# Performance work log

Hardware: AMD Instinct MI355X
Metric: run time of the kernel (lower is better)

Reference implementation:

```python
import jax, jax.numpy as jnp
import numpy as np

EPS = 1e-6
LAMBDA_INIT = 0.8

def rmsnorm(x, g):
    return x * jax.lax.rsqrt(jnp.mean(x * x, axis=-1, keepdims=True) + EPS) * g

def diff_attention(q_in, kv_in, Wq, Wk, Wv, Wo, lq1, lk1, lq2, lk2, causal):
    # q_in: [B,T,D], kv_in: [B,S,D]; Wq/Wk: [D, H*2*hs], Wv: [D, H*hs], Wo: [H*hs, D]
    B, T, _ = q_in.shape
    S = kv_in.shape[1]
    H, hs = lq1.shape
    q = (q_in @ Wq).reshape(B, T, H, 2, hs)
    k = (kv_in @ Wk).reshape(B, S, H, 2, hs)
    v = (kv_in @ Wv).reshape(B, S, H, hs)
    q1, q2 = q[..., 0, :], q[..., 1, :]
    k1, k2 = k[..., 0, :], k[..., 1, :]
    scale = 1.0 / np.sqrt(hs).astype(np.float32)
    a1 = jnp.einsum('bthd,bshd->bhts', q1, k1) * scale  # [B,H,T,S]
    a2 = jnp.einsum('bthd,bshd->bhts', q2, k2) * scale
    if causal:
        mask = jnp.tril(jnp.ones((T, S), dtype=bool))
        neg = jnp.asarray(-1e9, a1.dtype)
        a1 = jnp.where(mask, a1, neg)
        a2 = jnp.where(mask, a2, neg)
    s1 = jax.nn.softmax(a1, axis=-1)
    s2 = jax.nn.softmax(a2, axis=-1)
    lam = jnp.exp(jnp.sum(lq1 * lk1, -1)) - jnp.exp(jnp.sum(lq2 * lk2, -1)) + LAMBDA_INIT  # [H]
    attn = s1 - lam[None, :, None, None] * s2
    o = jnp.einsum('bhts,bshd->bthd', attn, v)  # [B,T,H,hs]
    # per-head RMSNorm (no affine) scaled by (1 - lambda_init), per Diff Transformer
    o = o * jax.lax.rsqrt(jnp.mean(o * o, -1, keepdims=True) + EPS) * (1.0 - LAMBDA_INIT)
    return o.reshape(B, T, H * hs) @ Wo

def swiglu(x, W1, W2, W3):
    return (jax.nn.silu(x @ W1) * (x @ W2)) @ W3

def setup_inputs():
    B, T, D, H, hs = 4, 1024, 1024, 16, 64
    Dff = 4 * D
    ks = jax.random.split(jax.random.key(0), 24)
    w = lambda i, shape, s=0.02: (jax.random.normal(ks[i], shape, jnp.float32) * s)
    return {
        'x': jax.random.normal(ks[0], (B, T, D), jnp.float32),
        'encoder_output': jax.random.normal(ks[1], (B, T, D), jnp.float32),
        'Wq_s': w(2, (D, H * 2 * hs)), 'Wk_s': w(3, (D, H * 2 * hs)),
        'Wv_s': w(4, (D, H * hs)), 'Wo_s': w(5, (H * hs, D)),
        'lq1_s': w(6, (H, hs), 0.1), 'lk1_s': w(7, (H, hs), 0.1),
        'lq2_s': w(8, (H, hs), 0.1), 'lk2_s': w(9, (H, hs), 0.1),
        'Wq_c': w(10, (D, H * 2 * hs)), 'Wk_c': w(11, (D, H * 2 * hs)),
        'Wv_c': w(12, (D, H * hs)), 'Wo_c': w(13, (H * hs, D)),
        'lq1_c': w(14, (H, hs), 0.1), 'lk1_c': w(15, (H, hs), 0.1),
        'lq2_c': w(16, (H, hs), 0.1), 'lk2_c': w(17, (H, hs), 0.1),
        'g_rms': jnp.ones((D,), jnp.float32),
        'W1': w(18, (D, Dff)), 'W2': w(19, (D, Dff)), 'W3': w(20, (Dff, D)),
    }

def reference(x, encoder_output, Wq_s, Wk_s, Wv_s, Wo_s, lq1_s, lk1_s, lq2_s, lk2_s,
              Wq_c, Wk_c, Wv_c, Wo_c, lq1_c, lk1_c, lq2_c, lk2_c,
              g_rms, W1, W2, W3):
    # dropout prob 0.0 -> identity (eval/reference mode)
    h = rmsnorm(x, g_rms)
    h = diff_attention(h, h, Wq_s, Wk_s, Wv_s, Wo_s, lq1_s, lk1_s, lq2_s, lk2_s, causal=True) + h
    h = diff_attention(h, encoder_output, Wq_c, Wk_c, Wv_c, Wo_c, lq1_c, lk1_c, lq2_c, lk2_c, causal=False)
    h = h + h  # faithful to source: out = dropout(out) + out after cross-attention
    h = swiglu(rmsnorm(h, g_rms), W1, W2, W3) + h
    return h
```

## Files before the change

kernel.cpp:

```cpp
#include <hip/hip_runtime.h>

typedef __attribute__((ext_vector_type(8))) short s16x8;
typedef __attribute__((ext_vector_type(4))) float f32x4;
typedef unsigned short u16;

__device__ __forceinline__ float bu2f(u16 u) {
    union { unsigned int i; float f; } x; x.i = ((unsigned int)u) << 16; return x.f;
}
__device__ __forceinline__ u16 f2bu(float f) {
    union { float f; unsigned int i; } x; x.f = f;
    unsigned int r = x.i + 0x7fffu + ((x.i >> 16) & 1u);
    return (u16)(r >> 16);
}

__device__ __forceinline__ void gld_lds16(const void* g, void* l) {
    __builtin_amdgcn_global_load_lds(
        (const __attribute__((address_space(1))) unsigned int*)g,
        (__attribute__((address_space(3))) unsigned int*)l, 16, 0, 0);
}
#define WAIT_VM0()   asm volatile("s_waitcnt vmcnt(0)" ::: "memory")
#define WAIT_LGKM0() asm volatile("s_waitcnt lgkmcnt(0)" ::: "memory")
#define RAW_BARRIER() asm volatile("s_barrier" ::: "memory")
#define MEMBAR()     asm volatile("" ::: "memory")

__global__ __launch_bounds__(256)
void transpose4_k(const float* s0, const float* s1, const float* s2, const float* s3,
                  u16* d0, u16* d1, u16* d2, u16* d3, int R, int C) {
    const float* src = blockIdx.z == 0 ? s0 : blockIdx.z == 1 ? s1 : blockIdx.z == 2 ? s2 : s3;
    u16* dst = blockIdx.z == 0 ? d0 : blockIdx.z == 1 ? d1 : blockIdx.z == 2 ? d2 : d3;
    __shared__ u16 t[32][33];
    int bx = blockIdx.x * 32, by = blockIdx.y * 32;
    int x = bx + threadIdx.x;
#pragma unroll
    for (int k = 0; k < 4; ++k)
        t[threadIdx.y + k * 8][threadIdx.x] = f2bu(src[(size_t)(by + threadIdx.y + k * 8) * C + x]);
    __syncthreads();
    int x2 = by + threadIdx.x;
#pragma unroll
    for (int k = 0; k < 4; ++k)
        dst[(size_t)(bx + threadIdx.y + k * 8) * R + x2] = t[threadIdx.x][threadIdx.y + k * 8];
}

__global__ __launch_bounds__(256)
void convert_k(const float* __restrict__ a, u16* __restrict__ o, int n4) {
    int i = blockIdx.x * 256 + threadIdx.x;
    if (i >= n4) return;
    float4 v = ((const float4*)a)[i];
    ushort4 u;
    u.x = f2bu(v.x); u.y = f2bu(v.y); u.z = f2bu(v.z); u.w = f2bu(v.w);
    ((ushort4*)o)[i] = u;
}

__global__ __launch_bounds__(256)
void rmsnorm_k(const float* __restrict__ x, const float* __restrict__ g, u16* __restrict__ y) {
    const int row = blockIdx.x, tid = threadIdx.x;
    float4 v = ((const float4*)(x + (size_t)row * 1024))[tid];
    float ss = v.x * v.x + v.y * v.y + v.z * v.z + v.w * v.w;
#pragma unroll
    for (int off = 32; off; off >>= 1) ss += __shfl_xor(ss, off, 64);
    __shared__ float red[4];
    if ((tid & 63) == 0) red[tid >> 6] = ss;
    __syncthreads();
    float tot = red[0] + red[1] + red[2] + red[3];
    float sc = rsqrtf(tot * (1.f / 1024.f) + 1e-6f);
    float4 gv = ((const float4*)g)[tid];
    ushort4 o;
    o.x = f2bu(v.x * sc * gv.x);
    o.y = f2bu(v.y * sc * gv.y);
    o.z = f2bu(v.z * sc * gv.z);
    o.w = f2bu(v.w * sc * gv.w);
    ((ushort4*)(y + (size_t)row * 1024))[tid] = o;
}

__global__ __launch_bounds__(256)
void silumul_k(const u16* __restrict__ a, const u16* __restrict__ b, u16* __restrict__ o, int n4) {
    int i = blockIdx.x * 256 + threadIdx.x;
    if (i >= n4) return;
    ushort4 ua = ((const ushort4*)a)[i], ub = ((const ushort4*)b)[i];
    ushort4 uo;
    {
        float v = bu2f(ua.x); uo.x = f2bu(v / (1.f + __expf(-v)) * bu2f(ub.x));
        v = bu2f(ua.y); uo.y = f2bu(v / (1.f + __expf(-v)) * bu2f(ub.y));
        v = bu2f(ua.z); uo.z = f2bu(v / (1.f + __expf(-v)) * bu2f(ub.z));
        v = bu2f(ua.w); uo.w = f2bu(v / (1.f + __expf(-v)) * bu2f(ub.w));
    }
    ((ushort4*)o)[i] = uo;
}

template <int TM>
__global__ __launch_bounds__(256, 2)
void gemm_bt(const u16* __restrict__ A, const u16* __restrict__ Bt, void* __restrict__ C,
             const void* __restrict__ res, int M, int N, int K, int mode) {
    constexpr int MI = TM / 32;
    __shared__ u16 sA[2][TM * 32];
    __shared__ u16 sB[2][128 * 32];
    const int tid = threadIdx.x;
    const int w = tid >> 6, lane = tid & 63, q4 = lane >> 4, l16 = lane & 15;
    const int m0 = blockIdx.y * TM, n0 = blockIdx.x * 128;
    const int wm = (w >> 1) * (TM / 2), wn = (w & 1) * 64;

    const f32x4 fzero = {0.f, 0.f, 0.f, 0.f};
    f32x4 acc[MI][4];
#pragma unroll
    for (int i = 0; i < MI; ++i)
#pragma unroll
        for (int j = 0; j < 4; ++j) acc[i][j] = fzero;

    const int r0 = tid >> 2, c0 = (tid & 3) * 8;

    auto stage = [&](int buf, int k0) {
        gld_lds16(A + (size_t)(m0 + r0) * K + k0 + c0, &sA[buf][tid * 8]);
        if (TM == 128)
            gld_lds16(A + (size_t)(m0 + 64 + r0) * K + k0 + c0, &sA[buf][(256 + tid) * 8]);
        gld_lds16(Bt + (size_t)(n0 + r0) * K + k0 + c0, &sB[buf][tid * 8]);
        gld_lds16(Bt + (size_t)(n0 + 64 + r0) * K + k0 + c0, &sB[buf][(256 + tid) * 8]);
    };

    const int nk = K >> 5;
    stage(0, 0);
    for (int it = 0; it < nk; ++it) {
        WAIT_VM0();
        RAW_BARRIER();
        if (it + 1 < nk) stage((it + 1) & 1, (it + 1) * 32);
        const int buf = it & 1;
        s16x8 af[MI], bfr[4];
#pragma unroll
        for (int i = 0; i < MI; ++i) af[i] = *(const s16x8*)&sA[buf][(wm + i * 16 + l16) * 32 + q4 * 8];
#pragma unroll
        for (int j = 0; j < 4; ++j) bfr[j] = *(const s16x8*)&sB[buf][(wn + j * 16 + l16) * 32 + q4 * 8];
#pragma unroll
        for (int i = 0; i < MI; ++i)
#pragma unroll
            for (int j = 0; j < 4; ++j)
                acc[i][j] = __builtin_amdgcn_mfma_f32_16x16x32_bf16(af[i], bfr[j], acc[i][j], 0, 0, 0);
        MEMBAR();
    }

    const size_t QBSZ = (size_t)4096 * 2048;
    const size_t FSZ  = (size_t)4096 * 4096;
#pragma unroll
    for (int i = 0; i < MI; ++i)
#pragma unroll
        for (int j = 0; j < 4; ++j)
#pragma unroll
            for (int r = 0; r < 4; ++r) {
                int m = m0 + wm + i * 16 + q4 * 4 + r;
                int n = n0 + wn + j * 16 + l16;
                float v = acc[i][j][r];
                if (mode == 0) {
                    ((u16*)C)[(size_t)m * N + n] = f2bu(v);
                } else if (mode == 1) {
                    ((u16*)C)[(size_t)m * N + n] = f2bu(v + bu2f(((const u16*)res)[(size_t)m * N + n]));
                } else if (mode == 2) {
                    ((float*)C)[(size_t)m * N + n] = 2.f * v;
                } else if (mode == 4) {
                    ((float*)C)[(size_t)m * N + n] = v + ((const float*)res)[(size_t)m * N + n];
                } else if (mode == 5) {
                    if (n < 2048) ((u16*)C)[(size_t)m * 2048 + n] = f2bu(v);
                    else if (n < 4096) ((u16*)C)[QBSZ + (size_t)m * 2048 + (n - 2048)] = f2bu(v);
                    else {
                        int nn = n - 4096, hh = nn >> 6, d = nn & 63, b = m >> 10, s = m & 1023;
                        ((u16*)C)[2 * QBSZ + ((size_t)((b * 16 + hh) * 64 + d)) * 1024 + s] = f2bu(v);
                    }
                } else if (mode == 6) {
                    if (n < 2048) ((u16*)C)[(size_t)m * 2048 + n] = f2bu(v);
                    else {
                        int nn = n - 2048, hh = nn >> 6, d = nn & 63, b = m >> 10, s = m & 1023;
                        ((u16*)C)[QBSZ + ((size_t)((b * 16 + hh) * 64 + d)) * 1024 + s] = f2bu(v);
                    }
                } else {
                    if (n < 4096) ((u16*)C)[(size_t)m * 4096 + n] = f2bu(v);
                    else ((u16*)C)[FSZ + (size_t)m * 4096 + (n - 4096)] = f2bu(v);
                }
            }
}

template <bool CAUSAL>
__global__ __launch_bounds__(256, 2)
void diff_flash(const u16* __restrict__ Q, const u16* __restrict__ Kg, const u16* __restrict__ Vt,
                u16* __restrict__ O, const float* __restrict__ lq1, const float* __restrict__ lk1,
                const float* __restrict__ lq2, const float* __restrict__ lk2, int T, int S) {
    __shared__ u16 sK1[2][64 * 64];
    __shared__ u16 sK2[2][64 * 64];
    __shared__ u16 sV[2][64 * 64];
    __shared__ u16 sP[4][16 * 64];

    const int tid = threadIdx.x;
    const int w = tid >> 6, lane = tid & 63, q4 = lane >> 4, l16 = lane & 15;
    const int h = blockIdx.x, b = blockIdx.y;
    const int zt = CAUSAL ? (gridDim.z - 1 - blockIdx.z) : blockIdx.z;
    const int t0 = zt * 64;
    const f32x4 fzero = {0.f, 0.f, 0.f, 0.f};

    float d1 = 0.f, d2 = 0.f;
    for (int d = 0; d < 64; ++d) {
        d1 += lq1[h * 64 + d] * lk1[h * 64 + d];
        d2 += lq2[h * 64 + d] * lk2[h * 64 + d];
    }
    const float lam = __expf(d1) - __expf(d2) + 0.8f;

    s16x8 qf[2][2];
    {
        const size_t qrow = (size_t)(b * T + t0 + w * 16 + l16) * 2048 + h * 128;
#pragma unroll
        for (int c = 0; c < 2; ++c)
#pragma unroll
            for (int kk = 0; kk < 2; ++kk)
                qf[c][kk] = *(const s16x8*)&Q[qrow + c * 64 + kk * 32 + q4 * 8];
    }

    f32x4 o1[4], o2[4];
    float ms1 = -1e30f, ls1 = 0.f, ms2 = -1e30f, ls2 = 0.f;
#pragma unroll
    for (int jn = 0; jn < 4; ++jn) { o1[jn] = fzero; o2[jn] = fzero; }

    const int ntiles = CAUSAL ? (zt + 1) : (S / 64);
    const int rk = tid >> 3;
    const int ckk = (((tid & 7) - rk) & 7) * 8;

    auto stage = [&](int buf, int s0) {
        const size_t kb = (size_t)(b * S + s0 + rk) * 2048 + h * 128;
        gld_lds16(&Kg[kb + ckk], &sK1[buf][tid * 8]);
        gld_lds16(&Kg[kb + (size_t)32 * 2048 + ckk], &sK1[buf][(256 + tid) * 8]);
        gld_lds16(&Kg[kb + 64 + ckk], &sK2[buf][tid * 8]);
        gld_lds16(&Kg[kb + (size_t)32 * 2048 + 64 + ckk], &sK2[buf][(256 + tid) * 8]);
        const size_t vb = (size_t)((b * 16 + h) * 64 + rk) * 1024 + s0;
        gld_lds16(&Vt[vb + ckk], &sV[buf][tid * 8]);
        gld_lds16(&Vt[vb + (size_t)32 * 1024 + ckk], &sV[buf][(256 + tid) * 8]);
    };

    u16* const sPw = sP[w];
    const int slot0 = ((0 * 4 + q4 + l16) & 7) * 8;
    const int slot1 = ((1 * 4 + q4 + l16) & 7) * 8;

    stage(0, 0);
    for (int it = 0; it < ntiles; ++it) {
        WAIT_VM0();
        RAW_BARRIER();
        if (it + 1 < ntiles) stage((it + 1) & 1, (it + 1) * 64);
        const int buf = it & 1, s0 = it * 64;
        const bool diag = CAUSAL && (it == ntiles - 1);

        s16x8 vf[4][2];
#pragma unroll
        for (int jn = 0; jn < 4; ++jn) {
            vf[jn][0] = *(const s16x8*)&sV[buf][(jn * 16 + l16) * 64 + slot0];
            vf[jn][1] = *(const s16x8*)&sV[buf][(jn * 16 + l16) * 64 + slot1];
        }

        auto comp_step = [&](const u16* sK, const s16x8* qkk, float& m, float& l, f32x4* o) {
            f32x4 sc[4];
#pragma unroll
            for (int js = 0; js < 4; ++js) sc[js] = fzero;
#pragma unroll
            for (int js = 0; js < 4; ++js) {
                s16x8 kf0 = *(const s16x8*)&sK[(js * 16 + l16) * 64 + slot0];
                sc[js] = __builtin_amdgcn_mfma_f32_16x16x32_bf16(kf0, qkk[0], sc[js], 0, 0, 0);
                s16x8 kf1 = *(const s16x8*)&sK[(js * 16 + l16) * 64 + slot1];
                sc[js] = __builtin_amdgcn_mfma_f32_16x16x32_bf16(kf1, qkk[1], sc[js], 0, 0, 0);
            }
            float p[4][4];
#pragma unroll
            for (int js = 0; js < 4; ++js)
#pragma unroll
                for (int r = 0; r < 4; ++r) {
                    float v = sc[js][r] * 0.125f;
                    if (diag && (s0 + js * 16 + q4 * 4 + r > t0 + w * 16 + l16)) v = -1e9f;
                    p[js][r] = v;
                }
            float mx = p[0][0];
#pragma unroll
            for (int js = 0; js < 4; ++js)
#pragma unroll
                for (int r = 0; r < 4; ++r) mx = fmaxf(mx, p[js][r]);
            mx = fmaxf(mx, __shfl_xor(mx, 16, 64));
            mx = fmaxf(mx, __shfl_xor(mx, 32, 64));
            float mn = fmaxf(m, mx);
            float alpha = __expf(m - mn);
            m = mn;
            float rs = 0.f;
#pragma unroll
            for (int js = 0; js < 4; ++js)
#pragma unroll
                for (int r = 0; r < 4; ++r) { p[js][r] = __expf(p[js][r] - mn); rs += p[js][r]; }
            rs += __shfl_xor(rs, 16, 64);
            rs += __shfl_xor(rs, 32, 64);
            l = l * alpha + rs;
#pragma unroll
            for (int jn = 0; jn < 4; ++jn) o[jn] *= alpha;
#pragma unroll
            for (int js = 0; js < 4; ++js) {
                ushort4 pk;
                pk.x = f2bu(p[js][0]); pk.y = f2bu(p[js][1]);
                pk.z = f2bu(p[js][2]); pk.w = f2bu(p[js][3]);
                int sl = ((js * 2 + (q4 >> 1) + l16) & 7) * 8 + (q4 & 1) * 4;
                *(ushort4*)&sPw[l16 * 64 + sl] = pk;
            }
            WAIT_LGKM0();
            s16x8 pb0 = *(const s16x8*)&sPw[l16 * 64 + slot0];
            s16x8 pb1 = *(const s16x8*)&sPw[l16 * 64 + slot1];
#pragma unroll
            for (int jn = 0; jn < 4; ++jn) {
                o[jn] = __builtin_amdgcn_mfma_f32_16x16x32_bf16(vf[jn][0], pb0, o[jn], 0, 0, 0);
                o[jn] = __builtin_amdgcn_mfma_f32_16x16x32_bf16(vf[jn][1], pb1, o[jn], 0, 0, 0);
            }
            MEMBAR();
        };
        comp_step(sK1[buf], qf[0], ms1, ls1, o1);
        comp_step(sK2[buf], qf[1], ms2, ls2, o2);
    }

    const float inv1 = 1.f / ls1, inv2 = lam / ls2;
    float val[4][4];
    float ss = 0.f;
#pragma unroll
    for (int jn = 0; jn < 4; ++jn)
#pragma unroll
        for (int r = 0; r < 4; ++r) {
            float v = o1[jn][r] * inv1 - o2[jn][r] * inv2;
            val[jn][r] = v;
            ss += v * v;
        }
    ss += __shfl_xor(ss, 16, 64);
    ss += __shfl_xor(ss, 32, 64);
    const float scl = rsqrtf(ss * (1.f / 64.f) + 1e-6f) * 0.2f;
    const size_t orow = (size_t)(b * T + t0 + w * 16 + l16) * 1024 + h * 64;
#pragma unroll
    for (int jn = 0; jn < 4; ++jn) {
        ushort4 ov;
        ov.x = f2bu(val[jn][0] * scl); ov.y = f2bu(val[jn][1] * scl);
        ov.z = f2bu(val[jn][2] * scl); ov.w = f2bu(val[jn][3] * scl);
        *(ushort4*)&O[orow + jn * 16 + q4 * 4] = ov;
    }
}

extern "C" void kernel_launch(void* const* d_in, const int* in_sizes, int n_in,
                              void* d_out, int out_size, void* d_ws, size_t ws_size,
                              hipStream_t stream) {
    (void)in_sizes; (void)n_in; (void)out_size; (void)ws_size;
    const float* x     = (const float*)d_in[0];
    const float* enc   = (const float*)d_in[1];
    const float* Wq_s  = (const float*)d_in[2];
    const float* Wk_s  = (const float*)d_in[3];
    const float* Wv_s  = (const float*)d_in[4];
    const float* Wo_s  = (const float*)d_in[5];
    const float* lq1_s = (const float*)d_in[6];
    const float* lk1_s = (const float*)d_in[7];
    const float* lq2_s = (const float*)d_in[8];
    const float* lk2_s = (const float*)d_in[9];
    const float* Wq_c  = (const float*)d_in[10];
    const float* Wk_c  = (const float*)d_in[11];
    const float* Wv_c  = (const float*)d_in[12];
    const float* Wo_c  = (const float*)d_in[13];
    const float* lq1_c = (const float*)d_in[14];
    const float* lk1_c = (const float*)d_in[15];
    const float* lq2_c = (const float*)d_in[16];
    const float* lk2_c = (const float*)d_in[17];
    const float* g_rms = (const float*)d_in[18];
    const float* W1    = (const float*)d_in[19];
    const float* W2    = (const float*)d_in[20];
    const float* W3    = (const float*)d_in[21];

    char* ws = (char*)d_ws;
    size_t off = 0;
    auto ab = [&](size_t elems) -> u16* { u16* p = (u16*)(ws + off); off += elems * 2; return p; };
    u16* WqkvTs = ab((size_t)5120 * 1024);
    u16* WoTs   = ab((size_t)1024 * 1024);
    u16* WqTc   = ab((size_t)2048 * 1024);
    u16* WkvTc  = ab((size_t)3072 * 1024);
    u16* WoTc   = ab((size_t)1024 * 1024);
    u16* W12T   = ab((size_t)8192 * 1024);
    u16* W3T    = ab((size_t)1024 * 4096);
    char* pool = ws + off;
    u16* h0   = ab((size_t)4096 * 1024);
    u16* encb = ab((size_t)4096 * 1024);
    u16* Qb   = ab((size_t)4096 * 2048);
    u16* Kb   = ab((size_t)4096 * 2048);
    u16* Vt   = ab((size_t)4096 * 1024);
    u16* Ob   = ab((size_t)4096 * 1024);
    u16* fa   = (u16*)pool;
    u16* fb   = (u16*)(pool + (size_t)4096 * 4096 * 2);
    u16* h1   = ab((size_t)4096 * 1024);
    float* h2 = (float*)(ws + off); off += (size_t)4096 * 1024 * 4;
    u16* rn   = ab((size_t)4096 * 1024);

    dim3 tb(32, 8);
    transpose4_k<<<dim3(64, 32, 4), tb, 0, stream>>>(
        Wq_s, Wk_s, Wq_c, Wk_c,
        WqkvTs, WqkvTs + (size_t)2048 * 1024, WqTc, WkvTc, 1024, 2048);
    transpose4_k<<<dim3(32, 32, 4), tb, 0, stream>>>(
        Wv_s, Wo_s, Wv_c, Wo_c,
        WqkvTs + (size_t)4096 * 1024, WoTs, WkvTc + (size_t)2048 * 1024, WoTc, 1024, 1024);
    transpose4_k<<<dim3(128, 32, 2), tb, 0, stream>>>(
        W1, W2, W1, W2, W12T, W12T + (size_t)4096 * 1024, W12T, W12T, 1024, 4096);
    transpose4_k<<<dim3(32, 128, 1), tb, 0, stream>>>(W3, W3, W3, W3, W3T, W3T, W3T, W3T, 4096, 1024);

    rmsnorm_k<<<4096, 256, 0, stream>>>(x, g_rms, h0);
    convert_k<<<4096, 256, 0, stream>>>(enc, encb, 4096 * 1024 / 4);

    gemm_bt<128><<<dim3(40, 32), 256, 0, stream>>>(h0, WqkvTs, Qb, nullptr, 4096, 5120, 1024, 5);
    diff_flash<true><<<dim3(16, 4, 16), 256, 0, stream>>>(Qb, Kb, Vt, Ob, lq1_s, lk1_s, lq2_s, lk2_s, 1024, 1024);
    gemm_bt<64><<<dim3(8, 64), 256, 0, stream>>>(Ob, WoTs, h1, h0, 4096, 1024, 1024, 1);

    gemm_bt<128><<<dim3(16, 32), 256, 0, stream>>>(h1, WqTc, Qb, nullptr, 4096, 2048, 1024, 0);
    gemm_bt<128><<<dim3(24, 32), 256, 0, stream>>>(encb, WkvTc, Kb, nullptr, 4096, 3072, 1024, 6);
    diff_flash<false><<<dim3(16, 4, 16), 256, 0, stream>>>(Qb, Kb, Vt, Ob, lq1_c, lk1_c, lq2_c, lk2_c, 1024, 1024);
    gemm_bt<64><<<dim3(8, 64), 256, 0, stream>>>(Ob, WoTc, h2, nullptr, 4096, 1024, 1024, 2);

    rmsnorm_k<<<4096, 256, 0, stream>>>(h2, g_rms, rn);
    gemm_bt<128><<<dim3(64, 32), 256, 0, stream>>>(rn, W12T, fa, nullptr, 4096, 8192, 1024, 7);
    silumul_k<<<16384, 256, 0, stream>>>(fa, fb, fa, 4096 * 4096 / 4);
    gemm_bt<64><<<dim3(8, 64), 256, 0, stream>>>(fa, W3T, (float*)d_out, h2, 4096, 1024, 4096, 4);
}
```

Before: 754.3 us.

## Register-staged double-buffer GEMM prefetch with compile-time K

Replaces the direct global-to-LDS loads and the wait-all-then-barrier loop in the bf16 GEMM with a register-staged pipeline. Global loads are issued two iterations ahead into registers and written to the other LDS buffer while MFMAs run on the current one. K becomes a template parameter, so addressing is constant and the loop can be fully specialized. The aim is to hide global memory latency behind compute, at the cost of more VGPRs, which may lower occupancy under launch_bounds(256,2).

```diff
diff --git a/kernel.cpp b/kernel.cpp
--- a/kernel.cpp
+++ b/kernel.cpp
@@ -17,6 +17,9 @@
     __builtin_amdgcn_global_load_lds(
         (const __attribute__((address_space(1))) unsigned int*)g,
         (__attribute__((address_space(3))) unsigned int*)l, 16, 0, 0);
+}
+__device__ __forceinline__ s16x8 ld16g(const u16* p) {
+    return *(const s16x8*)__builtin_assume_aligned(p, 16);
 }
 #define WAIT_VM0()   asm volatile("s_waitcnt vmcnt(0)" ::: "memory")
 #define WAIT_LGKM0() asm volatile("s_waitcnt lgkmcnt(0)" ::: "memory")
@@ -87,11 +90,13 @@
     ((ushort4*)o)[i] = uo;
 }
 
-template <int TM>
+template <int TM, int KK>
 __global__ __launch_bounds__(256, 2)
 void gemm_bt(const u16* __restrict__ A, const u16* __restrict__ Bt, void* __restrict__ C,
-             const void* __restrict__ res, int M, int N, int K, int mode) {
+             const void* __restrict__ res, int M, int N, int mode) {
     constexpr int MI = TM / 32;
+    constexpr int NA = TM / 64;
+    constexpr int nk = KK >> 5;
     __shared__ u16 sA[2][TM * 32];
     __shared__ u16 sB[2][128 * 32];
     const int tid = threadIdx.x;
@@ -107,33 +112,44 @@
         for (int j = 0; j < 4; ++j) acc[i][j] = fzero;
 
     const int r0 = tid >> 2, c0 = (tid & 3) * 8;
-
-    auto stage = [&](int buf, int k0) {
-        gld_lds16(A + (size_t)(m0 + r0) * K + k0 + c0, &sA[buf][tid * 8]);
-        if (TM == 128)
-            gld_lds16(A + (size_t)(m0 + 64 + r0) * K + k0 + c0, &sA[buf][(256 + tid) * 8]);
-        gld_lds16(Bt + (size_t)(n0 + r0) * K + k0 + c0, &sB[buf][tid * 8]);
-        gld_lds16(Bt + (size_t)(n0 + 64 + r0) * K + k0 + c0, &sB[buf][(256 + tid) * 8]);
+    const u16* apg = A + (size_t)(m0 + r0) * KK + c0;
+    const u16* bpg = Bt + (size_t)(n0 + r0) * KK + c0;
+
+    s16x8 ra[2][NA], rb[2][2];
+    auto gload = [&](int set, int it) {
+        const int k0 = it * 32;
+#pragma unroll
+        for (int i = 0; i < NA; ++i) ra[set][i] = ld16g(apg + k0 + (size_t)i * 64 * KK);
+        rb[set][0] = ld16g(bpg + k0);
+        rb[set][1] = ld16g(bpg + k0 + (size_t)64 * KK);
     };
-
-    const int nk = K >> 5;
-    stage(0, 0);
+    auto swrite = [&](int buf, int set) {
+#pragma unroll
+        for (int i = 0; i < NA; ++i) *(s16x8*)&sA[buf][(i * 256 + tid) * 8] = ra[set][i];
+        *(s16x8*)&sB[buf][tid * 8] = rb[set][0];
+        *(s16x8*)&sB[buf][(256 + tid) * 8] = rb[set][1];
+    };
+
+    gload(0, 0);
+    gload(1, 1);
+    swrite(0, 0);
+    __syncthreads();
+
     for (int it = 0; it < nk; ++it) {
-        WAIT_VM0();
-        RAW_BARRIER();
-        if (it + 1 < nk) stage((it + 1) & 1, (it + 1) * 32);
         const int buf = it & 1;
         s16x8 af[MI], bfr[4];
 #pragma unroll
         for (int i = 0; i < MI; ++i) af[i] = *(const s16x8*)&sA[buf][(wm + i * 16 + l16) * 32 + q4 * 8];
 #pragma unroll
         for (int j = 0; j < 4; ++j) bfr[j] = *(const s16x8*)&sB[buf][(wn + j * 16 + l16) * 32 + q4 * 8];
+        if (it + 2 < nk) gload(it & 1, it + 2);
+        if (it + 1 < nk) swrite(buf ^ 1, (it + 1) & 1);
 #pragma unroll
         for (int i = 0; i < MI; ++i)
 #pragma unroll
             for (int j = 0; j < 4; ++j)
                 acc[i][j] = __builtin_amdgcn_mfma_f32_16x16x32_bf16(af[i], bfr[j], acc[i][j], 0, 0, 0);
-        MEMBAR();
+        if (it + 1 < nk) __syncthreads();
     }
 
     const size_t QBSZ = (size_t)4096 * 2048;
@@ -398,17 +414,17 @@
     rmsnorm_k<<<4096, 256, 0, stream>>>(x, g_rms, h0);
     convert_k<<<4096, 256, 0, stream>>>(enc, encb, 4096 * 1024 / 4);
 
-    gemm_bt<128><<<dim3(40, 32), 256, 0, stream>>>(h0, WqkvTs, Qb, nullptr, 4096, 5120, 1024, 5);
+    gemm_bt<128, 1024><<<dim3(40, 32), 256, 0, stream>>>(h0, WqkvTs, Qb, nullptr, 4096, 5120, 5);
     diff_flash<true><<<dim3(16, 4, 16), 256, 0, stream>>>(Qb, Kb, Vt, Ob, lq1_s, lk1_s, lq2_s, lk2_s, 1024, 1024);
-    gemm_bt<64><<<dim3(8, 64), 256, 0, stream>>>(Ob, WoTs, h1, h0, 4096, 1024, 1024, 1);
-
-    gemm_bt<128><<<dim3(16, 32), 256, 0, stream>>>(h1, WqTc, Qb, nullptr, 4096, 2048, 1024, 0);
-    gemm_bt<128><<<dim3(24, 32), 256, 0, stream>>>(encb, WkvTc, Kb, nullptr, 4096, 3072, 1024, 6);
+    gemm_bt<64, 1024><<<dim3(8, 64), 256, 0, stream>>>(Ob, WoTs, h1, h0, 4096, 1024, 1);
+
+    gemm_bt<128, 1024><<<dim3(16, 32), 256, 0, stream>>>(h1, WqTc, Qb, nullptr, 4096, 2048, 0);
+    gemm_bt<128, 1024><<<dim3(24, 32), 256, 0, stream>>>(encb, WkvTc, Kb, nullptr, 4096, 3072, 6);
     diff_flash<false><<<dim3(16, 4, 16), 256, 0, stream>>>(Qb, Kb, Vt, Ob, lq1_c, lk1_c, lq2_c, lk2_c, 1024, 1024);
-    gemm_bt<64><<<dim3(8, 64), 256, 0, stream>>>(Ob, WoTc, h2, nullptr, 4096, 1024, 1024, 2);
+    gemm_bt<64, 1024><<<dim3(8, 64), 256, 0, stream>>>(Ob, WoTc, h2, nullptr, 4096, 1024, 2);
 
     rmsnorm_k<<<4096, 256, 0, stream>>>(h2, g_rms, rn);
-    gemm_bt<128><<<dim3(64, 32), 256, 0, stream>>>(rn, W12T, fa, nullptr, 4096, 8192, 1024, 7);
+    gemm_bt<128, 1024><<<dim3(64, 32), 256, 0, stream>>>(rn, W12T, fa, nullptr, 4096, 8192, 7);
     silumul_k<<<16384, 256, 0, stream>>>(fa, fb, fa, 4096 * 4096 / 4);
-    gemm_bt<64><<<dim3(8, 64), 256, 0, stream>>>(fa, W3T, (float*)d_out, h2, 4096, 1024, 4096, 4);
-}
+    gemm_bt<64, 4096><<<dim3(8, 64), 256, 0, stream>>>(fa, W3T, (float*)d_out, h2, 4096, 1024, 4);
+}
```

Result: slower. 2.272 ms (+201.1%).
